# Optimization experiments

Hardware: AMD Instinct MI355X
Metric: run time of the kernel (lower is better)

Reference implementation:

```python
import jax, jax.numpy as jnp
import numpy as np

V, C, T_BLK, H, L = 65, 512, 256, 8, 8
HS = C // H
EPS = 1e-5


def _ln(x, g, b):
    m = jnp.mean(x, axis=-1, keepdims=True)
    v = jnp.mean((x - m) ** 2, axis=-1, keepdims=True)
    return (x - m) * jax.lax.rsqrt(v + EPS) * g + b


def setup_inputs() -> dict:
    key = jax.random.key(0)
    ks = jax.random.split(key, 16)
    B, T = 64, 256
    idx = jax.random.randint(ks[0], (B, T), 0, V)
    targets = jax.random.randint(ks[1], (B, T), 0, V)
    n = lambda k, shape, s: (jax.random.normal(k, shape, dtype=jnp.float32) * s)
    return {
        "idx": idx,
        "targets": targets,
        "tok_emb": n(ks[2], (V, C), 0.02),
        "pos_emb": n(ks[3], (T_BLK, C), 0.02),
        "ln1_g": jnp.ones((L, C), jnp.float32),
        "ln1_b": jnp.zeros((L, C), jnp.float32),
        "wq": n(ks[4], (L, C, C), (2.0 / C) ** 0.5),
        "wk": n(ks[5], (L, C, C), (2.0 / C) ** 0.5),
        "wv": n(ks[6], (L, C, C), (2.0 / C) ** 0.5),
        "wo": n(ks[7], (L, C, C), (2.0 / C) ** 0.5),
        "bo": jnp.zeros((L, C), jnp.float32),
        "ln2_g": jnp.ones((L, C), jnp.float32),
        "ln2_b": jnp.zeros((L, C), jnp.float32),
        "w1": n(ks[8], (L, C, 4 * C), (2.0 / C) ** 0.5),
        "b1": jnp.zeros((L, 4 * C), jnp.float32),
        "w2": n(ks[9], (L, 4 * C, C), (2.0 / (4 * C)) ** 0.5),
        "b2": jnp.zeros((L, C), jnp.float32),
        "lnf_g": jnp.ones((C,), jnp.float32),
        "lnf_b": jnp.zeros((C,), jnp.float32),
        "lm_w": n(ks[10], (C, V), (2.0 / C) ** 0.5),
        "lm_b": jnp.zeros((V,), jnp.float32),
    }


def _gpt_forward(tok_emb, pos_emb, ln1_g, ln1_b, wq, wk, wv, wo, bo,
                 ln2_g, ln2_b, w1, b1, w2, b2, lnf_g, lnf_b, lm_w, lm_b,
                 idx, targets):
    B, T = idx.shape
    x = tok_emb[idx] + pos_emb[:T]  # [B,T,C]
    causal = jnp.tril(jnp.ones((T, T), bool))
    scale = float(C) ** -0.5  # NOTE: scaled by n_embd, not head_size (faithful)
    for l in range(L):
        h = _ln(x, ln1_g[l], ln1_b[l])
        q = (h @ wq[l]).reshape(B, T, H, HS)
        k = (h @ wk[l]).reshape(B, T, H, HS)
        v = (h @ wv[l]).reshape(B, T, H, HS)
        scores = jnp.einsum('bthd,bshd->bhts', q, k) * scale
        scores = jnp.where(causal, scores, -jnp.inf)
        w = jax.nn.softmax(scores, axis=-1)
        attn = jnp.einsum('bhts,bshd->bthd', w, v).reshape(B, T, C)
        x = x + attn @ wo[l] + bo[l]
        h2 = _ln(x, ln2_g[l], ln2_b[l])
        x = x + jax.nn.relu(h2 @ w1[l] + b1[l]) @ w2[l] + b2[l]
    x = _ln(x, lnf_g, lnf_b)
    logits = (x @ lm_w + lm_b).reshape(B * T, V)
    logp = jax.nn.log_softmax(logits, axis=-1)
    tgt = targets.reshape(B * T)
    loss = -jnp.mean(jnp.take_along_axis(logp, tgt[:, None], axis=-1))
    return logits, loss


def reference(idx, targets, tok_emb, pos_emb, ln1_g, ln1_b, wq, wk, wv, wo, bo,
              ln2_g, ln2_b, w1, b1, w2, b2, lnf_g, lnf_b, lm_w, lm_b):
    return _gpt_forward(tok_emb, pos_emb, ln1_g, ln1_b, wq, wk, wv, wo, bo,
                        ln2_g, ln2_b, w1, b1, w2, b2, lnf_g, lnf_b, lm_w, lm_b,
                        idx, targets)
```

## Files before the change

### kernel.cpp

```cpp
#include <hip/hip_runtime.h>
#include <math.h>

#define V_SZ   65
#define C_DIM  512
#define T_SEQ  256
#define H_N    8
#define HS_D   64
#define L_N    8
#define N_TOK  16384
#define LN_EPS 1e-5f
#define SM_SCALE 0.044194173824159216f

typedef unsigned short ushortT;
typedef __attribute__((ext_vector_type(8))) short    short8;
typedef __attribute__((ext_vector_type(8))) ushortT  ushort8;
typedef __attribute__((ext_vector_type(4))) float    f32x4;

typedef __attribute__((address_space(3))) unsigned int        lds_uint;
typedef const __attribute__((address_space(1))) unsigned int  glob_uint;

__device__ inline ushortT f2bf(float f) {
    unsigned int u = __float_as_uint(f);
    u = (u + 0x7fffu + ((u >> 16) & 1u)) >> 16;
    return (ushortT)u;
}
__device__ inline float bf2f(ushortT u) {
    return __uint_as_float(((unsigned int)u) << 16);
}

__global__ void embed_kernel(const int* __restrict__ idx,
                             const float* __restrict__ tok,
                             const float* __restrict__ pos,
                             ushortT* __restrict__ x) {
    int i = blockIdx.x * blockDim.x + threadIdx.x;
    const int NC8 = N_TOK * C_DIM / 8;
    if (i >= NC8) return;
    int c8 = i % (C_DIM / 8);
    int n  = i / (C_DIM / 8);
    int t  = n % T_SEQ;
    int tk = idx[n];
    const float4* ta = (const float4*)&tok[(size_t)tk * C_DIM + c8 * 8];
    const float4* pa = (const float4*)&pos[(size_t)t  * C_DIM + c8 * 8];
    float4 a0 = ta[0], a1 = ta[1], p0 = pa[0], p1 = pa[1];
    ushort8 r;
    r[0] = f2bf(a0.x + p0.x); r[1] = f2bf(a0.y + p0.y);
    r[2] = f2bf(a0.z + p0.z); r[3] = f2bf(a0.w + p0.w);
    r[4] = f2bf(a1.x + p1.x); r[5] = f2bf(a1.y + p1.y);
    r[6] = f2bf(a1.z + p1.z); r[7] = f2bf(a1.w + p1.w);
    *(ushort8*)&x[(size_t)i * 8] = r;
}

__global__ __launch_bounds__(256) void tcast_kernel(const float* __restrict__ src,
                                                    ushortT* __restrict__ dst,
                                                    int K, int N) {
    __shared__ float tile[32][33];
    size_t lo = (size_t)blockIdx.z * K * N;
    int n0 = blockIdx.x * 32, k0 = blockIdx.y * 32;
    int tx = threadIdx.x & 31, ty = threadIdx.x >> 5;
    #pragma unroll
    for (int s = 0; s < 4; s++) {
        int kk = ty + s * 8;
        tile[kk][tx] = src[lo + (size_t)(k0 + kk) * N + n0 + tx];
    }
    __syncthreads();
    #pragma unroll
    for (int s = 0; s < 4; s++) {
        int nn = ty + s * 8;
        dst[lo + (size_t)(n0 + nn) * K + k0 + tx] = f2bf(tile[tx][nn]);
    }
}

__global__ __launch_bounds__(256) void lmcast_kernel(const float* __restrict__ w,
                                                     ushortT* __restrict__ dst) {
    int n = blockIdx.x;
    for (int k = threadIdx.x; k < C_DIM; k += 256)
        dst[(size_t)n * C_DIM + k] = (n < V_SZ) ? f2bf(w[(size_t)k * V_SZ + n]) : (ushortT)0;
}

__global__ __launch_bounds__(256) void ln_kernel(const ushortT* __restrict__ in,
                                                 const float* __restrict__ g,
                                                 const float* __restrict__ b,
                                                 ushortT* __restrict__ outv) {
    int wave = threadIdx.x >> 6;
    int lane = threadIdx.x & 63;
    int row  = blockIdx.x * 4 + wave;
    ushort8 raw = *(const ushort8*)&in[(size_t)row * C_DIM + lane * 8];
    float v[8];
    #pragma unroll
    for (int k = 0; k < 8; k++) v[k] = bf2f(raw[k]);
    float s = 0.f;
    #pragma unroll
    for (int k = 0; k < 8; k++) s += v[k];
    #pragma unroll
    for (int m = 32; m >= 1; m >>= 1) s += __shfl_xor(s, m, 64);
    float mean = s * (1.0f / C_DIM);
    float vs = 0.f;
    #pragma unroll
    for (int k = 0; k < 8; k++) { float d = v[k] - mean; vs += d * d; }
    #pragma unroll
    for (int m = 32; m >= 1; m >>= 1) vs += __shfl_xor(vs, m, 64);
    float rstd = rsqrtf(vs * (1.0f / C_DIM) + LN_EPS);
    float gv[8], bv[8];
    *(float4*)&gv[0] = *(const float4*)&g[lane * 8];
    *(float4*)&gv[4] = *(const float4*)&g[lane * 8 + 4];
    *(float4*)&bv[0] = *(const float4*)&b[lane * 8];
    *(float4*)&bv[4] = *(const float4*)&b[lane * 8 + 4];
    ushort8 pack;
    #pragma unroll
    for (int k = 0; k < 8; k++) pack[k] = f2bf((v[k] - mean) * rstd * gv[k] + bv[k]);
    *(ushort8*)&outv[(size_t)row * C_DIM + lane * 8] = pack;
}

template<int EPI>
__device__ __forceinline__ void gemm_core(const ushortT* __restrict__ A,
                                          const ushortT* __restrict__ Bt,
                                          const float* __restrict__ bias,
                                          void* __restrict__ outp,
                                          int N, int K,
                                          int mBase, int nBase) {
    __shared__ __align__(16) ushortT As[128 * 32];
    __shared__ __align__(16) ushortT Bs[128 * 32];
    const int tid = threadIdx.x;
    const int w = tid >> 6, lane = tid & 63;
    const int wr = w >> 1, wc = w & 1;
    const int l15 = lane & 15, lg = lane >> 4;
    const int srow = (lane >> 2);
    const int sslot = lane & 3;

    f32x4 acc[4][4];
    #pragma unroll
    for (int i = 0; i < 4; i++)
        #pragma unroll
        for (int j = 0; j < 4; j++)
            acc[i][j] = {0.f, 0.f, 0.f, 0.f};

    for (int k0 = 0; k0 < K; k0 += 32) {
        #pragma unroll
        for (int t = 0; t < 2; t++) {
            int r = w * 32 + t * 16 + srow;
            int ks = sslot ^ ((r >> 1) & 3);
            const ushortT* ga = &A[(size_t)(mBase + r) * K + k0 + ks * 8];
            __builtin_amdgcn_global_load_lds((glob_uint*)ga,
                (lds_uint*)&As[(w * 32 + t * 16) * 32], 16, 0, 0);
            const ushortT* gb = &Bt[(size_t)(nBase + r) * K + k0 + ks * 8];
            __builtin_amdgcn_global_load_lds((glob_uint*)gb,
                (lds_uint*)&Bs[(w * 32 + t * 16) * 32], 16, 0, 0);
        }
        __syncthreads();
        short8 af[4], bfr[4];
        #pragma unroll
        for (int i = 0; i < 4; i++) {
            int r = wr * 64 + i * 16 + l15;
            int cb = (lg * 16) ^ (((r >> 1) & 3) << 4);
            af[i] = *(const short8*)((const char*)As + r * 64 + cb);
        }
        #pragma unroll
        for (int j = 0; j < 4; j++) {
            int r = wc * 64 + j * 16 + l15;
            int cb = (lg * 16) ^ (((r >> 1) & 3) << 4);
            bfr[j] = *(const short8*)((const char*)Bs + r * 64 + cb);
        }
        #pragma unroll
        for (int i = 0; i < 4; i++)
            #pragma unroll
            for (int j = 0; j < 4; j++)
                acc[i][j] = __builtin_amdgcn_mfma_f32_16x16x32_bf16(af[i], bfr[j], acc[i][j], 0, 0, 0);
        __syncthreads();
    }

    int lr = lg * 4;
    #pragma unroll
    for (int i = 0; i < 4; i++) {
        #pragma unroll
        for (int j = 0; j < 4; j++) {
            int col = nBase + wc * 64 + j * 16 + l15;
            if (EPI == 4 && col >= V_SZ) continue;
            #pragma unroll
            for (int q = 0; q < 4; q++) {
                size_t row = (size_t)(mBase + wr * 64 + i * 16 + lr + q);
                float vv = acc[i][j][q];
                if (EPI >= 2) vv += bias[col];
                if (EPI == 2) vv = fmaxf(vv, 0.f);
                if (EPI == 1)      ((ushortT*)outp)[row * N + col] = f2bf(vv);
                else if (EPI == 2) ((ushortT*)outp)[row * N + col] = f2bf(vv);
                else               ((float*)outp)[row * V_SZ + col] = vv;
            }
        }
    }
}

template<int EPI>
__global__ __launch_bounds__(256, 2) void gemm_bf16(const ushortT* __restrict__ A,
                                                    const ushortT* __restrict__ Bt,
                                                    const float* __restrict__ bias,
                                                    void* __restrict__ outp,
                                                    int N, int K) {
    gemm_core<EPI>(A, Bt, bias, outp, N, K, blockIdx.x * 128, blockIdx.y * 128);
}

__global__ __launch_bounds__(256, 2) void gemm_qkv(const ushortT* __restrict__ A,
                                                   const ushortT* __restrict__ bq,
                                                   const ushortT* __restrict__ bk,
                                                   const ushortT* __restrict__ bv,
                                                   ushortT* __restrict__ oq,
                                                   ushortT* __restrict__ ok,
                                                   ushortT* __restrict__ ov,
                                                   int N, int K) {
    const ushortT* Bt = (blockIdx.z == 0) ? bq : (blockIdx.z == 1) ? bk : bv;
    ushortT*       o  = (blockIdx.z == 0) ? oq : (blockIdx.z == 1) ? ok : ov;
    gemm_core<1>(A, Bt, nullptr, o, N, K, blockIdx.x * 128, blockIdx.y * 128);
}

__global__ __launch_bounds__(256, 2) void gemm_k64_res(const ushortT* __restrict__ A,
                                                       const ushortT* __restrict__ Bt,
                                                       const float* __restrict__ bias,
                                                       const ushortT* __restrict__ res,
                                                       ushortT* __restrict__ outp,
                                                       int N, int K) {
    __shared__ __align__(16) ushortT As[2][128 * 64];
    __shared__ __align__(16) ushortT Bs[2][128 * 64];
    const int tid = threadIdx.x;
    const int w = tid >> 6, lane = tid & 63;
    const int wr = w >> 1, wc = w & 1;
    const int l15 = lane & 15, lg = lane >> 4;
    const int mBase = blockIdx.x * 128, nBase = blockIdx.y * 128;
    const int NT = K >> 6;
    const int srow = lane >> 3;
    const int sgran = lane & 7;

    f32x4 acc[4][4];
    #pragma unroll
    for (int i = 0; i < 4; i++)
        #pragma unroll
        for (int j = 0; j < 4; j++)
            acc[i][j] = {0.f, 0.f, 0.f, 0.f};

    auto stage = [&](int buf, int k0) {
        #pragma unroll
        for (int t = 0; t < 4; t++) {
            int r = w * 32 + t * 8 + srow;
            int gl = sgran ^ (r & 7);
            const ushortT* ga = &A[(size_t)(mBase + r) * K + k0 + gl * 8];
            __builtin_amdgcn_global_load_lds((glob_uint*)ga,
                (lds_uint*)&As[buf][(w * 32 + t * 8) * 64], 16, 0, 0);
            const ushortT* gb = &Bt[(size_t)(nBase + r) * K + k0 + gl * 8];
            __builtin_amdgcn_global_load_lds((glob_uint*)gb,
                (lds_uint*)&Bs[buf][(w * 32 + t * 8) * 64], 16, 0, 0);
        }
    };

    stage(0, 0);
    int cur = 0;
    for (int t = 0; t < NT; t++) {
        asm volatile("s_waitcnt vmcnt(0)" ::: "memory");
        __builtin_amdgcn_s_barrier();
        __builtin_amdgcn_sched_barrier(0);
        if (t + 1 < NT) stage(cur ^ 1, (t + 1) * 64);

        const char* as = (const char*)&As[cur][0];
        const char* bs = (const char*)&Bs[cur][0];
        short8 af[2][4], bfr[2][4];
        #pragma unroll
        for (int i = 0; i < 4; i++) {
            int r = wr * 64 + i * 16 + l15;
            #pragma unroll
            for (int kk = 0; kk < 2; kk++) {
                int g = (kk * 4 + lg) ^ (r & 7);
                af[kk][i] = *(const short8*)(as + r * 128 + g * 16);
            }
        }
        #pragma unroll
        for (int j = 0; j < 4; j++) {
            int r = wc * 64 + j * 16 + l15;
            #pragma unroll
            for (int kk = 0; kk < 2; kk++) {
                int g = (kk * 4 + lg) ^ (r & 7);
                bfr[kk][j] = *(const short8*)(bs + r * 128 + g * 16);
            }
        }
        __builtin_amdgcn_s_setprio(1);
        #pragma unroll
        for (int kk = 0; kk < 2; kk++)
            #pragma unroll
            for (int i = 0; i < 4; i++)
                #pragma unroll
                for (int j = 0; j < 4; j++)
                    acc[i][j] = __builtin_amdgcn_mfma_f32_16x16x32_bf16(af[kk][i], bfr[kk][j], acc[i][j], 0, 0, 0);
        __builtin_amdgcn_s_setprio(0);
        asm volatile("s_waitcnt lgkmcnt(0)" ::: "memory");
        cur ^= 1;
    }

    int lr = lg * 4;
    #pragma unroll
    for (int i = 0; i < 4; i++) {
        #pragma unroll
        for (int j = 0; j < 4; j++) {
            int col = nBase + wc * 64 + j * 16 + l15;
            #pragma unroll
            for (int q = 0; q < 4; q++) {
                size_t row = (size_t)(mBase + wr * 64 + i * 16 + lr + q);
                float vv = acc[i][j][q] + bias[col] + bf2f(res[row * N + col]);
                outp[row * N + col] = f2bf(vv);
            }
        }
    }
}

__global__ __launch_bounds__(256) void attn_kernel(const ushortT* __restrict__ qp,
                                                   const ushortT* __restrict__ kp,
                                                   const ushortT* __restrict__ vp,
                                                   ushortT* __restrict__ att) {
    __shared__ ushortT K_lds[T_SEQ][72];
    __shared__ ushortT Vt_lds[HS_D][264];
    __shared__ ushortT P_lds[4][16][72];
    int bh = blockIdx.x;
    int b = bh >> 3, h = bh & 7;
    int tid = threadIdx.x;
    int w = tid >> 6, lane = tid & 63;
    const size_t rowbase = (size_t)b * T_SEQ * C_DIM + (size_t)h * HS_D;
    int l15 = lane & 15, lg = lane >> 4;

    #pragma unroll
    for (int it = 0; it < 8; it++) {
        int f = tid + it * 256;
        int r = f >> 3, c8 = f & 7;
        ushort8 kb = *(const ushort8*)&kp[rowbase + (size_t)r * C_DIM + c8 * 8];
        *(ushort8*)&K_lds[r][c8 * 8] = kb;
        ushort8 vb = *(const ushort8*)&vp[rowbase + (size_t)r * C_DIM + c8 * 8];
        #pragma unroll
        for (int e = 0; e < 8; e++) Vt_lds[c8 * 8 + e][r] = vb[e];
    }

    short8 qf[4][2];
    #pragma unroll
    for (int i = 0; i < 4; i++) {
        int grow = 16 * (4 * i + w) + l15;
        #pragma unroll
        for (int kk = 0; kk < 2; kk++)
            qf[i][kk] = *(const short8*)&qp[rowbase + (size_t)grow * C_DIM + kk * 32 + lg * 8];
    }
    __syncthreads();

    f32x4 acc_o[4][4];
    float mrun[4][4], lrun[4][4];
    #pragma unroll
    for (int i = 0; i < 4; i++) {
        #pragma unroll
        for (int j = 0; j < 4; j++) acc_o[i][j] = {0.f, 0.f, 0.f, 0.f};
        #pragma unroll
        for (int q = 0; q < 4; q++) { mrun[i][q] = -1e30f; lrun[i][q] = 0.f; }
    }

    #pragma unroll
    for (int jt = 0; jt < 4; jt++) {
        #pragma unroll
        for (int i = 0; i < 4; i++) {
            if (i < jt) continue;
            f32x4 acc_s[4];
            #pragma unroll
            for (int j_ = 0; j_ < 4; j_++) acc_s[j_] = {0.f, 0.f, 0.f, 0.f};
            #pragma unroll
            for (int j_ = 0; j_ < 4; j_++)
                #pragma unroll
                for (int kk = 0; kk < 2; kk++) {
                    short8 kf = *(const short8*)&K_lds[jt * 64 + j_ * 16 + l15][kk * 32 + lg * 8];
                    acc_s[j_] = __builtin_amdgcn_mfma_f32_16x16x32_bf16(qf[i][kk], kf, acc_s[j_], 0, 0, 0);
                }
            float sv[4][4];
            #pragma unroll
            for (int j_ = 0; j_ < 4; j_++) {
                int colg = jt * 64 + j_ * 16 + l15;
                #pragma unroll
                for (int q = 0; q < 4; q++) {
                    int rowg = 16 * (4 * i + w) + lg * 4 + q;
                    float s = acc_s[j_][q] * SM_SCALE;
                    sv[j_][q] = (i == jt && colg > rowg) ? -1e30f : s;
                }
            }
            #pragma unroll
            for (int q = 0; q < 4; q++) {
                float mx = fmaxf(fmaxf(sv[0][q], sv[1][q]), fmaxf(sv[2][q], sv[3][q]));
                #pragma unroll
                for (int msk = 1; msk <= 8; msk <<= 1) mx = fmaxf(mx, __shfl_xor(mx, msk, 64));
                float mold = mrun[i][q];
                float mnew = fmaxf(mold, mx);
                float corr = __expf(mold - mnew);
                mrun[i][q] = mnew;
                float ps = 0.f;
                #pragma unroll
                for (int j_ = 0; j_ < 4; j_++) {
                    float pe = __expf(sv[j_][q] - mnew);
                    ps += pe;
                    P_lds[w][lg * 4 + q][j_ * 16 + l15] = f2bf(pe);
                }
                lrun[i][q] = lrun[i][q] * corr + ps;
                #pragma unroll
                for (int dj = 0; dj < 4; dj++) acc_o[i][dj][q] *= corr;
            }
            short8 pa[2];
            #pragma unroll
            for (int kk = 0; kk < 2; kk++)
                pa[kk] = *(const short8*)&P_lds[w][l15][kk * 32 + lg * 8];
            #pragma unroll
            for (int dj = 0; dj < 4; dj++)
                #pragma unroll
                for (int kk = 0; kk < 2; kk++) {
                    short8 vf = *(const short8*)&Vt_lds[dj * 16 + l15][jt * 64 + kk * 32 + lg * 8];
                    acc_o[i][dj] = __builtin_amdgcn_mfma_f32_16x16x32_bf16(pa[kk], vf, acc_o[i][dj], 0, 0, 0);
                }
        }
    }

    #pragma unroll
    for (int i = 0; i < 4; i++) {
        float inv[4];
        #pragma unroll
        for (int q = 0; q < 4; q++) {
            float ls = lrun[i][q];
            #pragma unroll
            for (int msk = 1; msk <= 8; msk <<= 1) ls += __shfl_xor(ls, msk, 64);
            inv[q] = 1.0f / ls;
        }
        #pragma unroll
        for (int dj = 0; dj < 4; dj++) {
            int colg = dj * 16 + l15;
            #pragma unroll
            for (int q = 0; q < 4; q++) {
                int rowg = 16 * (4 * i + w) + lg * 4 + q;
                att[rowbase + (size_t)rowg * C_DIM + colg] = f2bf(acc_o[i][dj][q] * inv[q]);
            }
        }
    }
}

__global__ __launch_bounds__(256) void rowloss_kernel(const float* __restrict__ logits,
                                                      const int* __restrict__ tgt,
                                                      float* __restrict__ rl) {
    int wave = threadIdx.x >> 6, lane = threadIdx.x & 63;
    int n = blockIdx.x * 4 + wave;
    const float* l = logits + (size_t)n * V_SZ;
    float v0 = l[lane];
    float v1 = (lane == 0) ? l[64] : -1e30f;
    float m = fmaxf(v0, v1);
    #pragma unroll
    for (int s = 32; s >= 1; s >>= 1) m = fmaxf(m, __shfl_xor(m, s, 64));
    float e = __expf(v0 - m) + ((lane == 0) ? __expf(v1 - m) : 0.f);
    #pragma unroll
    for (int s = 32; s >= 1; s >>= 1) e += __shfl_xor(e, s, 64);
    if (lane == 0) {
        float lp = l[tgt[n]] - m - logf(e);
        rl[n] = -lp;
    }
}

__global__ __launch_bounds__(256) void reduce_loss_kernel(const float* __restrict__ rl,
                                                          float* __restrict__ out_loss) {
    __shared__ float sdata[256];
    float s = 0.f;
    for (int i = threadIdx.x; i < N_TOK; i += 256) s += rl[i];
    sdata[threadIdx.x] = s;
    __syncthreads();
    for (int st = 128; st > 0; st >>= 1) {
        if (threadIdx.x < st) sdata[threadIdx.x] += sdata[threadIdx.x + st];
        __syncthreads();
    }
    if (threadIdx.x == 0) out_loss[0] = sdata[0] * (1.0f / N_TOK);
}

extern "C" void kernel_launch(void* const* d_in, const int* in_sizes, int n_in,
                              void* d_out, int out_size, void* d_ws, size_t ws_size,
                              hipStream_t stream) {
    const int*   idx     = (const int*)d_in[0];
    const int*   targets = (const int*)d_in[1];
    const float* tok_emb = (const float*)d_in[2];
    const float* pos_emb = (const float*)d_in[3];
    const float* ln1_g   = (const float*)d_in[4];
    const float* ln1_b   = (const float*)d_in[5];
    const float* wq      = (const float*)d_in[6];
    const float* wk      = (const float*)d_in[7];
    const float* wv      = (const float*)d_in[8];
    const float* wo      = (const float*)d_in[9];
    const float* bo      = (const float*)d_in[10];
    const float* ln2_g   = (const float*)d_in[11];
    const float* ln2_b   = (const float*)d_in[12];
    const float* w1      = (const float*)d_in[13];
    const float* b1      = (const float*)d_in[14];
    const float* w2      = (const float*)d_in[15];
    const float* b2      = (const float*)d_in[16];
    const float* lnf_g   = (const float*)d_in[17];
    const float* lnf_b   = (const float*)d_in[18];
    const float* lm_w    = (const float*)d_in[19];
    const float* lm_b    = (const float*)d_in[20];

    float* out = (float*)d_out;
    char*  ws  = (char*)d_ws;
    const size_t MB = 1024ull * 1024ull;
    ushortT* x_bf  = (ushortT*)(ws);
    ushortT* h_bf  = (ushortT*)(ws + 32 * MB);
    ushortT* q_bf  = (ushortT*)(ws + 48 * MB);
    ushortT* k_bf  = (ushortT*)(ws + 64 * MB);
    ushortT* v_bf  = (ushortT*)(ws + 80 * MB);
    ushortT* att_bf= (ushortT*)(ws + 112 * MB);
    ushortT* ff1_bf= (ushortT*)(ws + 48 * MB);
    ushortT* wqT   = (ushortT*)(ws + 128 * MB);
    ushortT* wkT   = (ushortT*)(ws + 132 * MB);
    ushortT* wvT   = (ushortT*)(ws + 136 * MB);
    ushortT* woT   = (ushortT*)(ws + 140 * MB);
    ushortT* w1T   = (ushortT*)(ws + 144 * MB);
    ushortT* w2T   = (ushortT*)(ws + 160 * MB);
    float*   rl    = (float*)(ws + 176 * MB);
    ushortT* lmT   = (ushortT*)(ws + 177 * MB);

    {
        dim3 gCC(C_DIM / 32, C_DIM / 32, L_N);
        tcast_kernel<<<gCC, 256, 0, stream>>>(wq, wqT, C_DIM, C_DIM);
        tcast_kernel<<<gCC, 256, 0, stream>>>(wk, wkT, C_DIM, C_DIM);
        tcast_kernel<<<gCC, 256, 0, stream>>>(wv, wvT, C_DIM, C_DIM);
        tcast_kernel<<<gCC, 256, 0, stream>>>(wo, woT, C_DIM, C_DIM);
        dim3 g1(4 * C_DIM / 32, C_DIM / 32, L_N);
        tcast_kernel<<<g1, 256, 0, stream>>>(w1, w1T, C_DIM, 4 * C_DIM);
        dim3 g2(C_DIM / 32, 4 * C_DIM / 32, L_N);
        tcast_kernel<<<g2, 256, 0, stream>>>(w2, w2T, 4 * C_DIM, C_DIM);
        lmcast_kernel<<<128, 256, 0, stream>>>(lm_w, lmT);
    }

    embed_kernel<<<(N_TOK * C_DIM / 8 + 255) / 256, 256, 0, stream>>>(idx, tok_emb, pos_emb, x_bf);

    dim3 gemmCC(N_TOK / 128, C_DIM / 128);
    dim3 gemmC4(N_TOK / 128, 4 * C_DIM / 128);
    dim3 gemmQKV(N_TOK / 128, C_DIM / 128, 3);

    for (int l = 0; l < L_N; l++) {
        const ushortT* wqT_l = wqT + (size_t)l * C_DIM * C_DIM;
        const ushortT* wkT_l = wkT + (size_t)l * C_DIM * C_DIM;
        const ushortT* wvT_l = wvT + (size_t)l * C_DIM * C_DIM;
        const ushortT* woT_l = woT + (size_t)l * C_DIM * C_DIM;
        const ushortT* w1T_l = w1T + (size_t)l * C_DIM * 4 * C_DIM;
        const ushortT* w2T_l = w2T + (size_t)l * C_DIM * 4 * C_DIM;

        ln_kernel<<<N_TOK / 4, 256, 0, stream>>>(x_bf, ln1_g + l * C_DIM, ln1_b + l * C_DIM, h_bf);
        gemm_qkv<<<gemmQKV, 256, 0, stream>>>(h_bf, wqT_l, wkT_l, wvT_l, q_bf, k_bf, v_bf, C_DIM, C_DIM);
        attn_kernel<<<64 * H_N, 256, 0, stream>>>(q_bf, k_bf, v_bf, att_bf);
        gemm_k64_res<<<gemmCC, 256, 0, stream>>>(att_bf, woT_l, bo + l * C_DIM, x_bf, x_bf, C_DIM, C_DIM);
        ln_kernel<<<N_TOK / 4, 256, 0, stream>>>(x_bf, ln2_g + l * C_DIM, ln2_b + l * C_DIM, h_bf);
        gemm_bf16<2><<<gemmC4, 256, 0, stream>>>(h_bf, w1T_l, b1 + (size_t)l * 4 * C_DIM, ff1_bf, 4 * C_DIM, C_DIM);
        gemm_k64_res<<<gemmCC, 256, 0, stream>>>(ff1_bf, w2T_l, b2 + l * C_DIM, x_bf, x_bf, C_DIM, 4 * C_DIM);
    }

    ln_kernel<<<N_TOK / 4, 256, 0, stream>>>(x_bf, lnf_g, lnf_b, h_bf);
    gemm_bf16<4><<<dim3(N_TOK / 128, 1), 256, 0, stream>>>(h_bf, lmT, lm_b, out, V_SZ, C_DIM);

    rowloss_kernel<<<N_TOK / 4, 256, 0, stream>>>(out, targets, rl);
    reduce_loss_kernel<<<1, 256, 0, stream>>>(rl, out + (size_t)N_TOK * V_SZ);
}
```

Baseline: 1.562 ms.

## Add 8-wave 256x128 triple-buffered GEMM kernel for FFN first layer

Replaces the generic gemm_bf16<2> used for the FFN up-projection with a dedicated 512-thread kernel computing 256x128 tiles. It uses a three-slot LDS ring filled by direct global-to-LDS loads, with explicit vmcnt waits, and splits the next-tile staging across the two k-substeps so loads overlap MFMA work. The larger tile is meant to raise operand reuse and hide memory latency. The cost is one block per CU from heavy LDS use (~144KB) and hand-tuned wait counts that must match the issued loads exactly.

```diff
diff --git a/kernel.cpp b/kernel.cpp
--- a/kernel.cpp
+++ b/kernel.cpp
@@ -301,6 +301,116 @@
             for (int q = 0; q < 4; q++) {
                 size_t row = (size_t)(mBase + wr * 64 + i * 16 + lr + q);
                 float vv = acc[i][j][q] + bias[col] + bf2f(res[row * N + col]);
+                outp[row * N + col] = f2bf(vv);
+            }
+        }
+    }
+}
+
+__device__ __forceinline__ void w1_stage_part(const ushortT* __restrict__ A,
+                                              const ushortT* __restrict__ Bt,
+                                              ushortT* aslot, ushortT* bslot,
+                                              int mBase, int nBase, int K, int k0,
+                                              int w, int lane, int part) {
+    #pragma unroll
+    for (int jj = 0; jj < 2; jj++) {
+        int j = part * 2 + jj;
+        int c = w * 64 + lane + j * 512;
+        int r = c >> 3;
+        int gl = (c & 7) ^ (r & 7);
+        const ushortT* ga = &A[(size_t)(mBase + r) * K + k0 + gl * 8];
+        __builtin_amdgcn_global_load_lds((glob_uint*)ga,
+            (lds_uint*)&aslot[(w * 64 + j * 512) * 8], 16, 0, 0);
+    }
+    {
+        int j = part;
+        int c = w * 64 + lane + j * 512;
+        int r = c >> 3;
+        int gl = (c & 7) ^ (r & 7);
+        const ushortT* gb = &Bt[(size_t)(nBase + r) * K + k0 + gl * 8];
+        __builtin_amdgcn_global_load_lds((glob_uint*)gb,
+            (lds_uint*)&bslot[(w * 64 + j * 512) * 8], 16, 0, 0);
+    }
+}
+
+__global__ __launch_bounds__(512, 1) void gemm_w1_8ph(const ushortT* __restrict__ A,
+                                                      const ushortT* __restrict__ Bt,
+                                                      const float* __restrict__ bias,
+                                                      ushortT* __restrict__ outp,
+                                                      int N, int K) {
+    __shared__ __align__(16) ushortT As[3][256 * 64];
+    __shared__ __align__(16) ushortT Bs[3][128 * 64];
+    const int tid = threadIdx.x;
+    const int w = tid >> 6, lane = tid & 63;
+    const int wm = w >> 1, wn = w & 1;
+    const int l15 = lane & 15, lg = lane >> 4;
+    const int mBase = blockIdx.x * 256, nBase = blockIdx.y * 128;
+    const int NT = K >> 6;
+
+    f32x4 acc[4][4];
+    #pragma unroll
+    for (int i = 0; i < 4; i++)
+        #pragma unroll
+        for (int j = 0; j < 4; j++)
+            acc[i][j] = {0.f, 0.f, 0.f, 0.f};
+
+    #pragma unroll
+    for (int tt = 0; tt < 3; tt++) {
+        w1_stage_part(A, Bt, As[tt], Bs[tt], mBase, nBase, K, tt * 64, w, lane, 0);
+        w1_stage_part(A, Bt, As[tt], Bs[tt], mBase, nBase, K, tt * 64, w, lane, 1);
+    }
+
+    for (int t = 0; t < NT; t++) {
+        if (t == 0)          asm volatile("s_waitcnt vmcnt(12)" ::: "memory");
+        else if (t + 1 < NT) asm volatile("s_waitcnt vmcnt(6)" ::: "memory");
+        else                 asm volatile("s_waitcnt vmcnt(0)" ::: "memory");
+        __builtin_amdgcn_s_barrier();
+
+        const char* as = (const char*)&As[t % 3][0];
+        const char* bs = (const char*)&Bs[t % 3][0];
+        const bool st = (t + 2 < NT);
+        const int sslot = (t + 2) % 3, sk0 = (t + 2) * 64;
+
+        #pragma unroll
+        for (int kk = 0; kk < 2; kk++) {
+            short8 af[4], bfr[4];
+            #pragma unroll
+            for (int fr = 0; fr < 4; fr++) {
+                int r = wm * 64 + fr * 16 + l15;
+                int g = (kk * 4 + lg) ^ (r & 7);
+                af[fr] = *(const short8*)(as + r * 128 + g * 16);
+            }
+            #pragma unroll
+            for (int fc = 0; fc < 4; fc++) {
+                int r = wn * 64 + fc * 16 + l15;
+                int g = (kk * 4 + lg) ^ (r & 7);
+                bfr[fc] = *(const short8*)(bs + r * 128 + g * 16);
+            }
+            if (st) w1_stage_part(A, Bt, As[sslot], Bs[sslot], mBase, nBase, K, sk0, w, lane, kk);
+            asm volatile("s_waitcnt lgkmcnt(0)" ::: "memory");
+            __builtin_amdgcn_sched_barrier(0);
+            __builtin_amdgcn_s_setprio(1);
+            #pragma unroll
+            for (int fr = 0; fr < 4; fr++)
+                #pragma unroll
+                for (int fc = 0; fc < 4; fc++)
+                    acc[fr][fc] = __builtin_amdgcn_mfma_f32_16x16x32_bf16(af[fr], bfr[fc], acc[fr][fc], 0, 0, 0);
+            __builtin_amdgcn_s_setprio(0);
+            if (kk == 0) __builtin_amdgcn_s_barrier();
+        }
+    }
+
+    int lr = lg * 4;
+    #pragma unroll
+    for (int fr = 0; fr < 4; fr++) {
+        #pragma unroll
+        for (int fc = 0; fc < 4; fc++) {
+            int col = nBase + wn * 64 + fc * 16 + l15;
+            #pragma unroll
+            for (int q = 0; q < 4; q++) {
+                size_t row = (size_t)(mBase + wm * 64 + fr * 16 + lr + q);
+                float vv = acc[fr][fc][q] + bias[col];
+                vv = fmaxf(vv, 0.f);
                 outp[row * N + col] = f2bf(vv);
             }
         }
@@ -528,7 +638,7 @@
     embed_kernel<<<(N_TOK * C_DIM / 8 + 255) / 256, 256, 0, stream>>>(idx, tok_emb, pos_emb, x_bf);
 
     dim3 gemmCC(N_TOK / 128, C_DIM / 128);
-    dim3 gemmC4(N_TOK / 128, 4 * C_DIM / 128);
+    dim3 gemmW1(N_TOK / 256, 4 * C_DIM / 128);
     dim3 gemmQKV(N_TOK / 128, C_DIM / 128, 3);
 
     for (int l = 0; l < L_N; l++) {
@@ -544,7 +654,7 @@
         attn_kernel<<<64 * H_N, 256, 0, stream>>>(q_bf, k_bf, v_bf, att_bf);
         gemm_k64_res<<<gemmCC, 256, 0, stream>>>(att_bf, woT_l, bo + l * C_DIM, x_bf, x_bf, C_DIM, C_DIM);
         ln_kernel<<<N_TOK / 4, 256, 0, stream>>>(x_bf, ln2_g + l * C_DIM, ln2_b + l * C_DIM, h_bf);
-        gemm_bf16<2><<<gemmC4, 256, 0, stream>>>(h_bf, w1T_l, b1 + (size_t)l * 4 * C_DIM, ff1_bf, 4 * C_DIM, C_DIM);
+        gemm_w1_8ph<<<gemmW1, 512, 0, stream>>>(h_bf, w1T_l, b1 + (size_t)l * 4 * C_DIM, ff1_bf, 4 * C_DIM, C_DIM);
         gemm_k64_res<<<gemmCC, 256, 0, stream>>>(ff1_bf, w2T_l, b2 + l * C_DIM, x_bf, x_bf, C_DIM, 4 * C_DIM);
     }
 
```

Result: slower. 1.605 ms (+2.8%).
